# Optimization experiments

Measured on AMD Instinct MI355X. Metric: run time of the kernel, lower is better.

Reference implementation:

```python
import jax, jax.numpy as jnp
import numpy as np

ALPHA = 0.5  # torch forward default alpha


def setup_inputs() -> dict:
    key = jax.random.key(0)
    k1, k2, k3 = jax.random.split(key, 3)
    N, D, C = 16384, 2048, 1000
    group_x = jax.random.normal(k1, (N, D), dtype=jnp.float32)
    mu = jax.random.normal(k2, (C, D), dtype=jnp.float32)
    group_y = jax.random.randint(k3, (N,), 0, C, dtype=jnp.int64)
    return {"group_x": group_x, "group_y": group_y, "mu": mu}


def reference(group_x, group_y, mu):
    # Mahalanobis-style distance from original m_distance:
    # sqrt( diag((x - mu_c)(x - mu_c)^T) / 2 ) == sqrt(||x - mu_c||^2 / 2)
    # Computed directly (O(N*D*C) GEMM) instead of the original's O(N^2*D*C)
    # full pairwise matmul + diagonal extraction -- identical math.
    C = mu.shape[0]
    x_sq = jnp.sum(group_x * group_x, axis=1, keepdims=True)        # [N,1]
    mu_sq = jnp.sum(mu * mu, axis=1)[None, :]                        # [1,C]
    cross = jnp.einsum('nd,cd->nc', group_x, mu)                     # [N,C]
    sq_dist = jnp.maximum(x_sq - 2.0 * cross + mu_sq, 0.0)           # [N,C]
    distance = jnp.sqrt(sq_dist * 0.5)                               # [N,C]

    label_onehot = jax.nn.one_hot(group_y, C, dtype=distance.dtype)  # [N,C]
    adjust = distance * (1.0 + ALPHA * label_onehot)                 # [N,C]

    # F.cross_entropy(-adjust, group_y): mean NLL of log_softmax(-adjust)
    logp = jax.nn.log_softmax(-adjust, axis=1)                       # [N,C]
    picked = jnp.take_along_axis(logp, group_y[:, None], axis=1)[:, 0]
    return -jnp.mean(picked)
```

## Files before the change

### kernel.cpp

```cpp
#include <hip/hip_runtime.h>

typedef float f32x4  __attribute__((ext_vector_type(4)));
typedef int   i32x4  __attribute__((ext_vector_type(4)));
typedef int   i32x8  __attribute__((ext_vector_type(8)));

__device__ inline void gload_lds16(const void* g, void* l) {
    __builtin_amdgcn_global_load_lds((const __attribute__((address_space(1))) void*)g,
                                     (__attribute__((address_space(3))) void*)l,
                                     16, 0, 0);
}

__device__ inline unsigned int enc_fp4(float v) {
    float a = fabsf(v);
    unsigned int c = (unsigned int)(a > 0.25f) + (a > 0.75f) + (a > 1.25f) +
                     (a > 1.75f) + (a > 2.5f)  + (a > 3.5f)  + (a > 5.0f);
    return c | ((v < 0.f) ? 8u : 0u);
}

__global__ __launch_bounds__(256) void convert_kernel(
        const float* __restrict__ x, const float* __restrict__ mu,
        unsigned int* __restrict__ x4, unsigned int* __restrict__ mu4,
        float* __restrict__ x_sq, float* __restrict__ mu_sq,
        int D, int N, int C, int Cpad) {
    const int bid = blockIdx.x;
    const int t = threadIdx.x;
    const bool isX = bid < N;
    const int r = isX ? bid : bid - N;

    unsigned int* out = (isX ? x4 : mu4) + (size_t)r * (D / 8) + t;
    if (!isX && r >= C) {
        *out = 0u;
        if (t == 0) mu_sq[r] = 0.f;
        return;
    }
    const float* src = (isX ? x + (size_t)r * D : mu + (size_t)r * D) + t * 8;
    float4 v0 = *(const float4*)(src);
    float4 v1 = *(const float4*)(src + 4);
    float acc = v0.x * v0.x + v0.y * v0.y + v0.z * v0.z + v0.w * v0.w
              + v1.x * v1.x + v1.y * v1.y + v1.z * v1.z + v1.w * v1.w;
    unsigned int p = enc_fp4(v0.x) | (enc_fp4(v0.y) << 4) | (enc_fp4(v0.z) << 8)
                   | (enc_fp4(v0.w) << 12) | (enc_fp4(v1.x) << 16)
                   | (enc_fp4(v1.y) << 20) | (enc_fp4(v1.z) << 24)
                   | (enc_fp4(v1.w) << 28);
    *out = p;

    for (int off = 32; off; off >>= 1) acc += __shfl_down(acc, off, 64);
    __shared__ float sbuf[4];
    if ((t & 63) == 0) sbuf[t >> 6] = acc;
    __syncthreads();
    if (t == 0) {
        float s = sbuf[0] + sbuf[1] + sbuf[2] + sbuf[3];
        if (isX) x_sq[r] = s; else mu_sq[r] = s;
    }
}

#define BM 128
#define BN 256

__global__ __launch_bounds__(512, 4) void gemm_fused_kernel(
        const unsigned char* __restrict__ A,
        const unsigned char* __restrict__ B,
        const float* __restrict__ x_sq, const float* __restrict__ mu_sq,
        const int* __restrict__ y,
        float* __restrict__ pM, float* __restrict__ pS, float* __restrict__ pP,
        int Kb, int C, int NCB) {
    __shared__ __align__(16) char smem[49152];

    const int t  = threadIdx.x;
    const int l  = t & 63, w = t >> 6;
    const int wr = w >> 2, wc = w & 3;
    const int lr = l & 15, kh = l >> 4;
    const int rowBase = blockIdx.x * BM;
    const int colBase = blockIdx.y * BN;
    const int nt = Kb / 64;

    const int lc = (t & 3) ^ ((t >> 2) & 3);
    const unsigned char* gA = A + (size_t)(rowBase + (t >> 2)) * Kb + lc * 16;
    const unsigned char* gB = B + (size_t)(colBase + (t >> 2)) * Kb + lc * 16;

    auto STAGE = [&](int q) {
        const int qc = (q < nt) ? q : nt - 1;
        char* dst = smem + (q & 1) * 24576 + t * 16;
        const size_t ko = (size_t)qc * 64;
        gload_lds16(gA + ko, dst);
#pragma unroll
        for (int r = 0; r < 2; ++r)
            gload_lds16(gB + ko + (size_t)r * 128 * Kb, dst + 8192 + r * 8192);
    };

    const int pch = (kh ^ (lr & 3)) << 4;
    const int aBase = (wr * 64 + lr) * 64 + pch;
    const int bBase = 8192 + (wc * 64 + lr) * 64 + pch;

    f32x4 acc[4][4];
#pragma unroll
    for (int m = 0; m < 4; ++m)
#pragma unroll
        for (int n = 0; n < 4; ++n) acc[m][n] = (f32x4){0.f, 0.f, 0.f, 0.f};

    STAGE(0);
    asm volatile("s_waitcnt vmcnt(0)" ::: "memory");
    __builtin_amdgcn_s_barrier();

    const int SC = 0x7f7f7f7f;

#pragma unroll 2
    for (int q = 0; q < nt; ++q) {
        STAGE(q + 1);
        const char* buf = smem + (q & 1) * 24576;
        i32x4 aF[4], bF[4];
#pragma unroll
        for (int m = 0; m < 4; ++m)
            aF[m] = *(const i32x4*)(buf + aBase + m * 1024);
#pragma unroll
        for (int n = 0; n < 4; ++n)
            bF[n] = *(const i32x4*)(buf + bBase + n * 1024);
#pragma unroll
        for (int m = 0; m < 4; ++m) {
            i32x8 a8 = __builtin_shufflevector(aF[m], aF[m], 0, 1, 2, 3, -1, -1, -1, -1);
#pragma unroll
            for (int n = 0; n < 4; ++n) {
                i32x8 b8 = __builtin_shufflevector(bF[n], bF[n], 0, 1, 2, 3, -1, -1, -1, -1);
                acc[m][n] = __builtin_amdgcn_mfma_scale_f32_16x16x128_f8f6f4(
                    a8, b8, acc[m][n], 4 , 4 , 0, SC, 0, SC);
            }
        }
        asm volatile("s_waitcnt vmcnt(0)" ::: "memory");
        __builtin_amdgcn_s_barrier();
    }

    __syncthreads();
    float (*part)[4][3] = (float(*)[4][3])smem;

#pragma unroll
    for (int m = 0; m < 4; ++m) {
#pragma unroll
        for (int j = 0; j < 4; ++j) {
            const int row_l = wr * 64 + m * 16 + kh * 4 + j;
            const int grow = rowBase + row_l;
            const float xs = x_sq[grow];
            const int yr = y[grow];
            float v[4];
            float vmax = -3.4e38f, pick = -1.f;
#pragma unroll
            for (int n = 0; n < 4; ++n) {
                const int col = colBase + wc * 64 + n * 16 + lr;
                const float cr = acc[m][n][j];
                const float sq = fmaxf(xs - 2.f * cr + mu_sq[col], 0.f) * 0.5f;
                const float dd = sqrtf(sq);
                const float adj = (col == yr) ? 1.5f * dd : dd;
                if (col == yr) pick = adj;
                v[n] = (col < C) ? -adj : -1e30f;
                vmax = fmaxf(vmax, v[n]);
            }
            for (int off = 1; off <= 8; off <<= 1)
                vmax = fmaxf(vmax, __shfl_xor(vmax, off, 64));
            float s = 0.f;
#pragma unroll
            for (int n = 0; n < 4; ++n) s += expf(v[n] - vmax);
            for (int off = 1; off <= 8; off <<= 1) s += __shfl_xor(s, off, 64);
            for (int off = 1; off <= 8; off <<= 1)
                pick = fmaxf(pick, __shfl_xor(pick, off, 64));
            if (lr == 0) {
                part[row_l][wc][0] = vmax;
                part[row_l][wc][1] = s;
                part[row_l][wc][2] = pick;
            }
        }
    }
    __syncthreads();
    if (t < 128) {
        float Mx = part[t][0][0], S = 0.f, pk = part[t][0][2];
#pragma unroll
        for (int b = 1; b < 4; ++b) Mx = fmaxf(Mx, part[t][b][0]);
#pragma unroll
        for (int b = 0; b < 4; ++b) {
            S += part[t][b][1] * expf(part[t][b][0] - Mx);
            pk = fmaxf(pk, part[t][b][2]);
        }
        const size_t o = (size_t)(rowBase + t) * NCB + blockIdx.y;
        pM[o] = Mx; pS[o] = S; pP[o] = pk;
    }
}

__global__ __launch_bounds__(256) void loss_combine_kernel(
        const float* __restrict__ pM, const float* __restrict__ pS,
        const float* __restrict__ pP, float* __restrict__ bsum, int NCB) {
    const int t = threadIdx.x;
    const int row = blockIdx.x * 256 + t;
    float Mx = -3.4e38f;
    for (int b = 0; b < NCB; ++b) Mx = fmaxf(Mx, pM[(size_t)row * NCB + b]);
    float S = 0.f, pick = -1.f;
    for (int b = 0; b < NCB; ++b) {
        S += pS[(size_t)row * NCB + b] * expf(pM[(size_t)row * NCB + b] - Mx);
        pick = fmaxf(pick, pP[(size_t)row * NCB + b]);
    }
    float loss = pick + logf(S) + Mx;
    for (int off = 32; off; off >>= 1) loss += __shfl_down(loss, off, 64);
    __shared__ float sb[4];
    if ((t & 63) == 0) sb[t >> 6] = loss;
    __syncthreads();
    if (t == 0) bsum[blockIdx.x] = sb[0] + sb[1] + sb[2] + sb[3];
}

__global__ __launch_bounds__(64) void final_mean_kernel(
        const float* __restrict__ bsum, float* __restrict__ out, int nb, int N) {
    float a = 0.f;
    for (int i = threadIdx.x; i < nb; i += 64) a += bsum[i];
    for (int off = 32; off; off >>= 1) a += __shfl_down(a, off, 64);
    if (threadIdx.x == 0) out[0] = a / (float)N;
}

extern "C" void kernel_launch(void* const* d_in, const int* in_sizes, int n_in,
                              void* d_out, int out_size, void* d_ws, size_t ws_size,
                              hipStream_t stream) {
    const float* x  = (const float*)d_in[0];
    const int*   y  = (const int*)d_in[1];
    const float* mu = (const float*)d_in[2];

    const int N = in_sizes[1];
    const int D = in_sizes[0] / N;
    const int C = in_sizes[2] / D;
    const int Cpad = ((C + 255) / 256) * 256;
    const int NCB = Cpad / BN;
    const int NRB = N / 256;
    const int Kb = D / 2;

    char* ws = (char*)d_ws;
    unsigned char* x4  = (unsigned char*)ws;  ws += (size_t)N * Kb;
    unsigned char* mu4 = (unsigned char*)ws;  ws += (size_t)Cpad * Kb;
    float* x_sq  = (float*)ws;                ws += (size_t)N * 4;
    float* mu_sq = (float*)ws;                ws += (size_t)Cpad * 4;
    float* pM    = (float*)ws;                ws += (size_t)N * NCB * 4;
    float* pS    = (float*)ws;                ws += (size_t)N * NCB * 4;
    float* pP    = (float*)ws;                ws += (size_t)N * NCB * 4;
    float* bsum  = (float*)ws;                ws += (size_t)NRB * 4;

    convert_kernel<<<N + Cpad, 256, 0, stream>>>(
        x, mu, (unsigned int*)x4, (unsigned int*)mu4, x_sq, mu_sq, D, N, C, Cpad);
    gemm_fused_kernel<<<dim3(N / BM, Cpad / BN), 512, 0, stream>>>(
        x4, mu4, x_sq, mu_sq, y, pM, pS, pP, Kb, C, NCB);
    loss_combine_kernel<<<NRB, 256, 0, stream>>>(pM, pS, pP, bsum, NCB);
    final_mean_kernel<<<1, 64, 0, stream>>>(bsum, d_out ? (float*)d_out : nullptr, NRB, N);
}
```

Baseline: 72.21 us.

## Fuse loss combine and mean reduction into GEMM via last-block atomics

Removes the separate loss_combine and final_mean kernels. Each GEMM block increments a per-row-panel counter, and the last block for a panel merges the column partials and adds a fixed-point row-loss sum to a global atomic. The final block writes the mean. The counters are reset in the convert kernel. This saves two kernel launches and the extra pass over the partials. In exchange it adds fences and atomics, a hardcoded partial count of 4, and fixed-point rounding of the loss.

```diff
diff --git a/kernel.cpp b/kernel.cpp
--- a/kernel.cpp
+++ b/kernel.cpp
@@ -21,9 +21,17 @@
         const float* __restrict__ x, const float* __restrict__ mu,
         unsigned int* __restrict__ x4, unsigned int* __restrict__ mu4,
         float* __restrict__ x_sq, float* __restrict__ mu_sq,
-        int D, int N, int C, int Cpad) {
+        int* __restrict__ panel_cnt, unsigned int* __restrict__ done_cnt,
+        unsigned long long* __restrict__ loss_sum,
+        int D, int N, int C, int Cpad, int NPAN) {
     const int bid = blockIdx.x;
     const int t = threadIdx.x;
+
+    if (t == 0 && bid < NPAN) {
+        panel_cnt[bid] = 0;
+        if (bid == 0) { *done_cnt = 0u; *loss_sum = 0ull; }
+    }
+
     const bool isX = bid < N;
     const int r = isX ? bid : bid - N;
 
@@ -63,6 +71,8 @@
         const float* __restrict__ x_sq, const float* __restrict__ mu_sq,
         const int* __restrict__ y,
         float* __restrict__ pM, float* __restrict__ pS, float* __restrict__ pP,
+        int* __restrict__ panel_cnt, unsigned int* __restrict__ done_cnt,
+        unsigned long long* __restrict__ loss_sum, float* __restrict__ outv,
         int Kb, int C, int NCB) {
     __shared__ __align__(16) char smem[49152];
 
@@ -181,34 +191,46 @@
         const size_t o = (size_t)(rowBase + t) * NCB + blockIdx.y;
         pM[o] = Mx; pS[o] = S; pP[o] = pk;
     }
-}
-
-__global__ __launch_bounds__(256) void loss_combine_kernel(
-        const float* __restrict__ pM, const float* __restrict__ pS,
-        const float* __restrict__ pP, float* __restrict__ bsum, int NCB) {
-    const int t = threadIdx.x;
-    const int row = blockIdx.x * 256 + t;
-    float Mx = -3.4e38f;
-    for (int b = 0; b < NCB; ++b) Mx = fmaxf(Mx, pM[(size_t)row * NCB + b]);
-    float S = 0.f, pick = -1.f;
-    for (int b = 0; b < NCB; ++b) {
-        S += pS[(size_t)row * NCB + b] * expf(pM[(size_t)row * NCB + b] - Mx);
-        pick = fmaxf(pick, pP[(size_t)row * NCB + b]);
-    }
-    float loss = pick + logf(S) + Mx;
-    for (int off = 32; off; off >>= 1) loss += __shfl_down(loss, off, 64);
-    __shared__ float sb[4];
-    if ((t & 63) == 0) sb[t >> 6] = loss;
-    __syncthreads();
-    if (t == 0) bsum[blockIdx.x] = sb[0] + sb[1] + sb[2] + sb[3];
-}
-
-__global__ __launch_bounds__(64) void final_mean_kernel(
-        const float* __restrict__ bsum, float* __restrict__ out, int nb, int N) {
-    float a = 0.f;
-    for (int i = threadIdx.x; i < nb; i += 64) a += bsum[i];
-    for (int off = 32; off; off >>= 1) a += __shfl_down(a, off, 64);
-    if (threadIdx.x == 0) out[0] = a / (float)N;
+
+    __threadfence();
+    __syncthreads();
+    __shared__ int lastFlag;
+    if (t == 0)
+        lastFlag = (atomicAdd(&panel_cnt[blockIdx.x], 1) == (int)gridDim.y - 1);
+    __syncthreads();
+    if (!lastFlag) return;
+    __threadfence();
+
+    int my = 0;
+    if (t < 128) {
+        const size_t rb = (size_t)(rowBase + t) * NCB;
+        float Mx = pM[rb];
+        for (int b = 1; b < 4; ++b) Mx = fmaxf(Mx, pM[rb + b]);
+        float S = 0.f, pick = -1.f;
+        for (int b = 0; b < 4; ++b) {
+            S += pS[rb + b] * expf(pM[rb + b] - Mx);
+            pick = fmaxf(pick, pP[rb + b]);
+        }
+        const float loss = pick + logf(S) + Mx;
+        my = (int)__float2int_rn(loss * 65536.0f);
+    }
+    for (int off = 32; off; off >>= 1) my += __shfl_down(my, off, 64);
+    __shared__ int isum[8];
+    if ((t & 63) == 0) isum[t >> 6] = my;
+    __syncthreads();
+    if (t == 0) {
+        long long bs = 0;
+#pragma unroll
+        for (int i = 0; i < 8; ++i) bs += isum[i];
+        atomicAdd(loss_sum, (unsigned long long)(long long)bs);
+        __threadfence();
+        if (atomicAdd(done_cnt, 1u) == gridDim.x - 1) {
+            __threadfence();
+            unsigned long long tot = atomicAdd(loss_sum, 0ull);
+            const double Nrows = (double)(gridDim.x * BM);
+            outv[0] = (float)((double)(long long)tot / 65536.0 / Nrows);
+        }
+    }
 }
 
 extern "C" void kernel_launch(void* const* d_in, const int* in_sizes, int n_in,
@@ -223,7 +245,7 @@
     const int C = in_sizes[2] / D;
     const int Cpad = ((C + 255) / 256) * 256;
     const int NCB = Cpad / BN;
-    const int NRB = N / 256;
+    const int NPAN = N / BM;
     const int Kb = D / 2;
 
     char* ws = (char*)d_ws;
@@ -234,12 +256,15 @@
     float* pM    = (float*)ws;                ws += (size_t)N * NCB * 4;
     float* pS    = (float*)ws;                ws += (size_t)N * NCB * 4;
     float* pP    = (float*)ws;                ws += (size_t)N * NCB * 4;
-    float* bsum  = (float*)ws;                ws += (size_t)NRB * 4;
+    unsigned long long* loss_sum = (unsigned long long*)ws; ws += 8;
+    unsigned int* done_cnt       = (unsigned int*)ws;       ws += 8;
+    int* panel_cnt               = (int*)ws;                ws += (size_t)NPAN * 4;
 
     convert_kernel<<<N + Cpad, 256, 0, stream>>>(
-        x, mu, (unsigned int*)x4, (unsigned int*)mu4, x_sq, mu_sq, D, N, C, Cpad);
+        x, mu, (unsigned int*)x4, (unsigned int*)mu4, x_sq, mu_sq,
+        panel_cnt, done_cnt, loss_sum, D, N, C, Cpad, NPAN);
     gemm_fused_kernel<<<dim3(N / BM, Cpad / BN), 512, 0, stream>>>(
-        x4, mu4, x_sq, mu_sq, y, pM, pS, pP, Kb, C, NCB);
-    loss_combine_kernel<<<NRB, 256, 0, stream>>>(pM, pS, pP, bsum, NCB);
-    final_mean_kernel<<<1, 64, 0, stream>>>(bsum, d_out ? (float*)d_out : nullptr, NRB, N);
-}
+        x4, mu4, x_sq, mu_sq, y, pM, pS, pP,
+        panel_cnt, done_cnt, loss_sum, d_out ? (float*)d_out : nullptr,
+        Kb, C, NCB);
+}
```

Measured after the change: 159.6 us. +121.0%, slower.
